# Kernel tuning notes

Hardware: AMD Instinct MI355X
Metric: run time of the kernel (lower is better)

## Reference

```python
import jax, jax.numpy as jnp
import numpy as np

B, T, C = 4, 1024, 1024
H, HKV, D = 16, 4, 64
GATE_CH = 12
ROPE_THETA = 10000.0


def _rms_norm(x):
    # F.rms_norm with default eps = machine epsilon of dtype, no learnable scale
    eps = jnp.finfo(x.dtype).eps
    ms = jnp.mean(jnp.square(x), axis=-1, keepdims=True)
    return x * jax.lax.rsqrt(ms + eps)


def _apply_rotary(x, cos, sin):
    # x: (B, T, h, D); cos/sin: (1, T, 1, D//2). Half-split rotation.
    d = x.shape[-1] // 2
    x1, x2 = x[..., :d], x[..., d:]
    y1 = x1 * cos + x2 * sin
    y2 = -x1 * sin + x2 * cos
    return jnp.concatenate([y1, y2], axis=-1)


def setup_inputs() -> dict:
    key = jax.random.key(0)
    ks = jax.random.split(key, 8)
    x = jax.random.normal(ks[0], (B, T, C), dtype=jnp.float32)
    ve = jax.random.normal(ks[1], (B, T, HKV * D), dtype=jnp.float32)
    # real RoPE tables, shape (1, T, 1, D//2)
    half = D // 2
    inv_freq = 1.0 / (ROPE_THETA ** (np.arange(half, dtype=np.float32) / half))
    freqs = np.arange(T, dtype=np.float32)[:, None] * inv_freq[None, :]
    cos = jnp.asarray(np.cos(freqs), dtype=jnp.float32).reshape(1, T, 1, half)
    sin = jnp.asarray(np.sin(freqs), dtype=jnp.float32).reshape(1, T, 1, half)
    s = 0.02
    Wq = jax.random.normal(ks[2], (H * D, C), dtype=jnp.float32) * s
    Wk = jax.random.normal(ks[3], (HKV * D, C), dtype=jnp.float32) * s
    Wv = jax.random.normal(ks[4], (HKV * D, C), dtype=jnp.float32) * s
    Wo = jax.random.normal(ks[5], (C, C), dtype=jnp.float32) * s
    Wg = jax.random.normal(ks[6], (HKV, GATE_CH), dtype=jnp.float32) * s
    return {"x": x, "ve": ve, "cos": cos, "sin": sin,
            "Wq": Wq, "Wk": Wk, "Wv": Wv, "Wo": Wo, "Wg": Wg,
            "window_size": 256}


def reference(x, ve, cos, sin, Wq, Wk, Wv, Wo, Wg, window_size):
    b, t, c = x.shape
    d = 2 * cos.shape[-1]
    h = Wq.shape[0] // d
    hkv = Wk.shape[0] // d
    rep = h // hkv

    q = (x @ Wq.T).reshape(b, t, h, d)
    k = (x @ Wk.T).reshape(b, t, hkv, d)
    v = (x @ Wv.T).reshape(b, t, hkv, d)

    # value-embedding sigmoid gate (3 * sigmoid of first 12 channels of x)
    gate = 3.0 * jax.nn.sigmoid(x[..., : Wg.shape[1]] @ Wg.T)  # (b, t, hkv)
    v = v + gate[..., None] * ve.reshape(b, t, hkv, d)

    q = _apply_rotary(q, cos, sin)
    k = _apply_rotary(k, cos, sin)
    q = _rms_norm(q) * 1.2
    k = _rms_norm(k) * 1.2

    # GQA attention with sliding-window causal mask (left=window_size, right=0)
    qg = q.reshape(b, t, hkv, rep, d)
    scale = 1.0 / jnp.sqrt(jnp.asarray(d, dtype=q.dtype))
    scores = jnp.einsum('bqgrd,bkgd->bgrqk', qg, k) * scale
    i = jnp.arange(t)[:, None]
    j = jnp.arange(t)[None, :]
    mask = (j <= i) & ((i - j) <= window_size)  # (t, t)
    scores = jnp.where(mask[None, None, None], scores, -jnp.inf)
    probs = jax.nn.softmax(scores, axis=-1)
    y = jnp.einsum('bgrqk,bkgd->bqgrd', probs, v).reshape(b, t, h * d)
    return y @ Wo.T
```

## Files before the change

### kernel.cpp

```cpp
#include <hip/hip_runtime.h>

typedef __bf16 v8bf __attribute__((ext_vector_type(8)));
typedef float v4f __attribute__((ext_vector_type(4)));
typedef unsigned int v4u __attribute__((ext_vector_type(4)));
typedef unsigned int v2u __attribute__((ext_vector_type(2)));
typedef unsigned short u16;

#define DEVI static __device__ __forceinline__

DEVI float bf2f(u16 u) {
    union { float f; unsigned int i; } c; c.i = ((unsigned int)u) << 16; return c.f;
}
DEVI u16 f2bf(float f) {
    union { float f; unsigned int i; } c; c.f = f;
    unsigned int i = c.i;
    i += 0x7fffu + ((i >> 16) & 1u);
    return (u16)(i >> 16);
}

union Frag { v4u u; v8bf v; u16 h[8]; };

#define GLD16(gptr, lptr) __builtin_amdgcn_global_load_lds( \
    (const __attribute__((address_space(1))) void*)(gptr),  \
    (__attribute__((address_space(3))) void*)(lptr), 16, 0, 0)

__global__ __launch_bounds__(256) void convert5(
    const float* __restrict__ x, const float* __restrict__ wq,
    const float* __restrict__ wk, const float* __restrict__ wv,
    const float* __restrict__ wo, u16* __restrict__ xb,
    u16* __restrict__ wb, u16* __restrict__ wob)
{
    const float* src; u16* dst; int n;
    switch (blockIdx.y) {
        case 0: src = x;  dst = xb;               n = 4096 * 1024; break;
        case 1: src = wq; dst = wb;               n = 1024 * 1024; break;
        case 2: src = wk; dst = wb + 1024 * 1024; n = 256 * 1024;  break;
        case 3: src = wv; dst = wb + 1280 * 1024; n = 256 * 1024;  break;
        default: src = wo; dst = wob;             n = 1024 * 1024; break;
    }
    const int stride = gridDim.x * 256 * 4;
    for (int i = (blockIdx.x * 256 + threadIdx.x) * 4; i < n; i += stride) {
        const float4 f = *(const float4*)(src + i);
        v2u p;
        p[0] = (unsigned int)f2bf(f.x) | ((unsigned int)f2bf(f.y) << 16);
        p[1] = (unsigned int)f2bf(f.z) | ((unsigned int)f2bf(f.w) << 16);
        *(v2u*)(dst + i) = p;
    }
}

template <bool F32OUT>
__global__ __launch_bounds__(256) void gemm_bt(
    const u16* __restrict__ A, const u16* __restrict__ B,
    void* __restrict__ Cv, int N)
{
    __shared__ __align__(16) u16 As[64 * 64];
    __shared__ __align__(16) u16 Bs[128 * 64];
    const int tid  = threadIdx.x;
    const int lane = tid & 63, l15 = lane & 15, quad = lane >> 4;
    const int w    = tid >> 6;
    const int wr   = (w >> 1) * 32, wc = (w & 1) * 64;
    const int m0   = blockIdx.y * 64, n0 = blockIdx.x * 128;

    const u16* ab = A + m0 * 1024;
    const u16* bb = B + n0 * 1024;

    const int r0 = tid >> 3;
    const int c0 = (tid & 7) * 8;
    const u16* ag = ab + r0 * 1024 + c0;
    const u16* bg = bb + r0 * 1024 + c0;
    u16* al = &As[r0 * 64 + c0];
    u16* bl = &Bs[r0 * 64 + c0];

    v4f acc[2][4];
    const v4f vzero = {0.f, 0.f, 0.f, 0.f};
#pragma unroll
    for (int i = 0; i < 2; i++)
#pragma unroll
        for (int j = 0; j < 4; j++) acc[i][j] = vzero;

    for (int k0 = 0; k0 < 1024; k0 += 64) {
        __syncthreads();
        GLD16(ag + k0,             al);
        GLD16(ag + k0 + 32 * 1024, al + 32 * 64);
        GLD16(bg + k0,             bl);
        GLD16(bg + k0 + 32 * 1024, bl + 32 * 64);
        GLD16(bg + k0 + 64 * 1024, bl + 64 * 64);
        GLD16(bg + k0 + 96 * 1024, bl + 96 * 64);
        __syncthreads();
#pragma unroll
        for (int ks = 0; ks < 2; ks++) {
            v8bf af[2];
#pragma unroll
            for (int mi = 0; mi < 2; mi++)
                af[mi] = *(const v8bf*)&As[(wr + mi * 16 + l15) * 64 + ks * 32 + quad * 8];
#pragma unroll
            for (int ni = 0; ni < 4; ni++) {
                v8bf bv = *(const v8bf*)&Bs[(wc + ni * 16 + l15) * 64 + ks * 32 + quad * 8];
#pragma unroll
                for (int mi = 0; mi < 2; mi++)
                    acc[mi][ni] = __builtin_amdgcn_mfma_f32_16x16x32_bf16(af[mi], bv, acc[mi][ni], 0, 0, 0);
            }
        }
    }
#pragma unroll
    for (int mi = 0; mi < 2; mi++) {
        const int row = m0 + wr + mi * 16 + quad * 4;
#pragma unroll
        for (int ni = 0; ni < 4; ni++) {
            const int col = n0 + wc + ni * 16 + l15;
#pragma unroll
            for (int r = 0; r < 4; r++) {
                if (F32OUT) ((float*)Cv)[(row + r) * N + col] = acc[mi][ni][r];
                else        ((u16*)Cv)[(row + r) * N + col] = f2bf(acc[mi][ni][r]);
            }
        }
    }
}

__global__ __launch_bounds__(256) void fixup(
    const u16* __restrict__ qkv, const float* __restrict__ x,
    const float* __restrict__ ve, const float* __restrict__ cs,
    const float* __restrict__ sn, const float* __restrict__ Wg,
    u16* __restrict__ qn, u16* __restrict__ kn, u16* __restrict__ vn)
{
    const int token = blockIdx.x;
    const int pos   = token & 1023;
    const int tid   = threadIdx.x;
    const int hw    = tid >> 5, l = tid & 31;
    const float c = cs[pos * 32 + l];
    const float s = sn[pos * 32 + l];
#pragma unroll
    for (int it = 0; it < 3; it++) {
        const int task = it * 8 + hw;
        if (task < 20) {
            const u16* src; u16* dst;
            if (task < 16) { src = qkv + token * 1536 + task * 64;               dst = qn + token * 1024 + task * 64; }
            else           { src = qkv + token * 1536 + 1024 + (task - 16) * 64; dst = kn + token * 256 + (task - 16) * 64; }
            const float x1 = bf2f(src[l]), x2 = bf2f(src[32 + l]);
            const float y1 = x1 * c + x2 * s;
            const float y2 = x2 * c - x1 * s;
            float ss = y1 * y1 + y2 * y2;
#pragma unroll
            for (int off = 16; off >= 1; off >>= 1) ss += __shfl_xor(ss, off, 64);
            const float inv = rsqrtf(ss * (1.0f / 64.0f) + 1.1920929e-7f) * 1.2f;
            dst[l]      = f2bf(y1 * inv);
            dst[32 + l] = f2bf(y2 * inv);
        } else {
            const int g = task - 20;
            float dot = 0.f;
#pragma unroll
            for (int cc = 0; cc < 12; cc++)
                dot += x[token * 1024 + cc] * Wg[g * 12 + cc];
            const float gate = 3.f / (1.f + __expf(-dot));
            const u16*   vsrc  = qkv + token * 1536 + 1280 + g * 64;
            const float* vesrc = ve + token * 256 + g * 64;
            u16* vdst = vn + token * 256 + g * 64;
            vdst[l]      = f2bf(bf2f(vsrc[l])      + gate * vesrc[l]);
            vdst[32 + l] = f2bf(bf2f(vsrc[32 + l]) + gate * vesrc[32 + l]);
        }
    }
}

__global__ __launch_bounds__(256) void vtrans(
    const u16* __restrict__ vn, u16* __restrict__ vt)
{
    __shared__ __align__(16) u16 T[64 * 72];
    const int tid = threadIdx.x;
    const int t0  = blockIdx.x * 64, g = blockIdx.y, b = blockIdx.z;
    {
        const int row = tid >> 2, ch = (tid & 3) * 16;
        const int goff = (b * 1024 + t0 + row) * 256 + g * 64 + ch;
        *(v4u*)&T[row * 72 + ch]     = *(const v4u*)&vn[goff];
        *(v4u*)&T[row * 72 + ch + 8] = *(const v4u*)&vn[goff + 8];
    }
    __syncthreads();
    {
        const int d = tid >> 2, tc = (tid & 3) * 16;
        Frag o0, o1;
#pragma unroll
        for (int j = 0; j < 8; j++) {
            o0.h[j] = T[(tc + j) * 72 + d];
            o1.h[j] = T[(tc + 8 + j) * 72 + d];
        }
        u16* dst = vt + ((b * 4 + g) * 64 + d) * 1024 + t0 + tc;
        *(v4u*)dst       = o0.u;
        *(v4u*)(dst + 8) = o1.u;
    }
}

__global__ __launch_bounds__(256) void attn(
    const u16* __restrict__ qn, const u16* __restrict__ kn,
    const u16* __restrict__ vt, u16* __restrict__ yo)
{
    __shared__ __align__(16) u16 Ks[64 * 72];
    __shared__ __align__(16) u16 VTs[64 * 72];
    __shared__ __align__(16) u16 Ps[4][16 * 72];
    const int tid  = threadIdx.x;
    const int w    = tid >> 6, lane = tid & 63, l15 = lane & 15, quad = lane >> 4;
    const int qb   = blockIdx.x, h = blockIdx.y, b = blockIdx.z;
    const int g    = h >> 2;
    const int qbase = qb * 64;
    const int qabs0 = qbase + w * 16;
    const int tok0  = b * 1024 + qabs0;
    u16* pw = Ps[w];

    v8bf qf[2];
#pragma unroll
    for (int ks = 0; ks < 2; ks++) {
        Frag f;
        f.u = *(const v4u*)&qn[(tok0 + l15) * 1024 + h * 64 + ks * 32 + quad * 8];
#pragma unroll
        for (int j = 0; j < 8; j++) f.h[j] = f2bf(0.125f * bf2f(f.h[j]));
        qf[ks] = f.v;
    }

    v4f o[4];
    float mi_[4], li_[4];
    const v4f vzero = {0.f, 0.f, 0.f, 0.f};
#pragma unroll
    for (int nd = 0; nd < 4; nd++) o[nd] = vzero;
#pragma unroll
    for (int r = 0; r < 4; r++) { mi_[r] = -1e30f; li_[r] = 0.f; }

    const int kstart = (qbase >= 256) ? qbase - 256 : 0;
    for (int kbase = kstart; kbase <= qbase; kbase += 64) {
        __syncthreads();
        {
            const int row = tid >> 2, ch = (tid & 3) * 16;
            const int goff = (b * 1024 + kbase + row) * 256 + g * 64 + ch;
            *(v4u*)&Ks[row * 72 + ch]     = *(const v4u*)&kn[goff];
            *(v4u*)&Ks[row * 72 + ch + 8] = *(const v4u*)&kn[goff + 8];
            const u16* vsrc = vt + ((b * 4 + g) * 64 + row) * 1024 + kbase + ch;
            *(v4u*)&VTs[row * 72 + ch]     = *(const v4u*)vsrc;
            *(v4u*)&VTs[row * 72 + ch + 8] = *(const v4u*)(vsrc + 8);
        }
        __syncthreads();

        bool skip[4], full[4];
#pragma unroll
        for (int ni = 0; ni < 4; ni++) {
            const int left = kbase + ni * 16;
            skip[ni] = (left > qabs0 + 15) || (qabs0 - (left + 15) > 256);
            full[ni] = ((left + 15) <= qabs0) && ((qabs0 + 15 - left) <= 256);
        }

        v4f sc[4];
        float rmax[4] = {-1e30f, -1e30f, -1e30f, -1e30f};
#pragma unroll
        for (int ni = 0; ni < 4; ni++) {
            if (skip[ni]) continue;
            v8bf kf0 = *(const v8bf*)&Ks[(ni * 16 + l15) * 72 + quad * 8];
            v8bf kf1 = *(const v8bf*)&Ks[(ni * 16 + l15) * 72 + 32 + quad * 8];
            v4f a = vzero;
            a = __builtin_amdgcn_mfma_f32_16x16x32_bf16(qf[0], kf0, a, 0, 0, 0);
            a = __builtin_amdgcn_mfma_f32_16x16x32_bf16(qf[1], kf1, a, 0, 0, 0);
            if (!full[ni]) {
                const int kj = kbase + ni * 16 + l15;
#pragma unroll
                for (int r = 0; r < 4; r++) {
                    const int qi = qabs0 + quad * 4 + r;
                    if (!((kj <= qi) && (qi - kj <= 256))) a[r] = -1e30f;
                }
            }
            sc[ni] = a;
#pragma unroll
            for (int r = 0; r < 4; r++) rmax[r] = fmaxf(rmax[r], a[r]);
        }
#pragma unroll
        for (int off = 8; off >= 1; off >>= 1)
#pragma unroll
            for (int r = 0; r < 4; r++)
                rmax[r] = fmaxf(rmax[r], __shfl_xor(rmax[r], off, 64));

        float mn[4], alp[4], ps[4];
#pragma unroll
        for (int r = 0; r < 4; r++) {
            mn[r]  = fmaxf(mi_[r], rmax[r]);
            alp[r] = __expf(mi_[r] - mn[r]);
            mi_[r] = mn[r];
            ps[r]  = 0.f;
        }
#pragma unroll
        for (int ni = 0; ni < 4; ni++) {
            if (skip[ni]) {
#pragma unroll
                for (int r = 0; r < 4; r++)
                    pw[(quad * 4 + r) * 72 + ni * 16 + l15] = 0;
            } else {
#pragma unroll
                for (int r = 0; r < 4; r++) {
                    const float p = __expf(sc[ni][r] - mn[r]);
                    ps[r] += p;
                    pw[(quad * 4 + r) * 72 + ni * 16 + l15] = f2bf(p);
                }
            }
        }
#pragma unroll
        for (int off = 8; off >= 1; off >>= 1)
#pragma unroll
            for (int r = 0; r < 4; r++)
                ps[r] += __shfl_xor(ps[r], off, 64);
#pragma unroll
        for (int r = 0; r < 4; r++)
            li_[r] = li_[r] * alp[r] + ps[r];
#pragma unroll
        for (int nd = 0; nd < 4; nd++)
#pragma unroll
            for (int r = 0; r < 4; r++)
                o[nd][r] *= alp[r];

#pragma unroll
        for (int ks = 0; ks < 2; ks++) {
            if (skip[2 * ks] && skip[2 * ks + 1]) continue;
            v8bf af = *(const v8bf*)&pw[l15 * 72 + ks * 32 + quad * 8];
#pragma unroll
            for (int nd = 0; nd < 4; nd++) {
                v8bf bv = *(const v8bf*)&VTs[(nd * 16 + l15) * 72 + ks * 32 + quad * 8];
                o[nd] = __builtin_amdgcn_mfma_f32_16x16x32_bf16(af, bv, o[nd], 0, 0, 0);
            }
        }
    }

    float inv[4];
#pragma unroll
    for (int r = 0; r < 4; r++) inv[r] = 1.f / li_[r];
#pragma unroll
    for (int nd = 0; nd < 4; nd++) {
        const int col = h * 64 + nd * 16 + l15;
#pragma unroll
        for (int r = 0; r < 4; r++) {
            const int row = tok0 + quad * 4 + r;
            yo[row * 1024 + col] = f2bf(o[nd][r] * inv[r]);
        }
    }
}

extern "C" void kernel_launch(void* const* d_in, const int* in_sizes, int n_in,
                              void* d_out, int out_size, void* d_ws, size_t ws_size,
                              hipStream_t stream)
{
    const float* x  = (const float*)d_in[0];
    const float* ve = (const float*)d_in[1];
    const float* cs = (const float*)d_in[2];
    const float* sn = (const float*)d_in[3];
    const float* Wq = (const float*)d_in[4];
    const float* Wk = (const float*)d_in[5];
    const float* Wv = (const float*)d_in[6];
    const float* Wo = (const float*)d_in[7];
    const float* Wg = (const float*)d_in[8];

    u16* xb  = (u16*)d_ws;
    u16* wb  = xb  + 4096 * 1024;
    u16* wob = wb  + 1536 * 1024;
    u16* qkv = wob + 1024 * 1024;
    u16* qn  = qkv + 4096 * 1536;
    u16* kn  = qn  + 4096 * 1024;
    u16* vn  = kn  + 4096 * 256;
    u16* vt  = vn  + 4096 * 256;
    u16* ay  = qkv;

    convert5<<<dim3(512, 5), 256, 0, stream>>>(x, Wq, Wk, Wv, Wo, xb, wb, wob);
    gemm_bt<false><<<dim3(12, 64), 256, 0, stream>>>(xb, wb, (void*)qkv, 1536);
    fixup<<<4096, 256, 0, stream>>>(qkv, x, ve, cs, sn, Wg, qn, kn, vn);
    vtrans<<<dim3(16, 4, 4), 256, 0, stream>>>(vn, vt);
    attn<<<dim3(16, 16, 4), 256, 0, stream>>>(qn, kn, vt, ay);
    gemm_bt<true><<<dim3(8, 64), 256, 0, stream>>>(ay, wob, d_out, 1024);
}
```

Before: 173.1 us.

## Fuse all stages into one cooperative persistent kernel with grid syncs

Replaces the six separate launches (convert, QKV GEMM, fixup, V transpose, attention, output GEMM) with a single cooperative kernel of 512 blocks. The stages are separated by grid.sync barriers. The V transpose is folded into the fixup stage through shared memory, which removes the vn intermediate buffer. The goal is to cut launch overhead and inter-kernel gaps. The cost is fixed 512-block parallelism, uneven work per stage (768 GEMM tiles over 512 blocks), grid-barrier latency, and an occupancy limit of 2 blocks per CU.

```diff
diff --git a/kernel.cpp b/kernel.cpp
--- a/kernel.cpp
+++ b/kernel.cpp
@@ -1,4 +1,7 @@
 #include <hip/hip_runtime.h>
+#include <hip/hip_cooperative_groups.h>
+
+namespace cg = cooperative_groups;
 
 typedef __bf16 v8bf __attribute__((ext_vector_type(8)));
 typedef float v4f __attribute__((ext_vector_type(4)));
@@ -24,46 +27,26 @@
     (const __attribute__((address_space(1))) void*)(gptr),  \
     (__attribute__((address_space(3))) void*)(lptr), 16, 0, 0)
 
-__global__ __launch_bounds__(256) void convert5(
-    const float* __restrict__ x, const float* __restrict__ wq,
-    const float* __restrict__ wk, const float* __restrict__ wv,
-    const float* __restrict__ wo, u16* __restrict__ xb,
-    u16* __restrict__ wb, u16* __restrict__ wob)
+DEVI void cvt4(const float* __restrict__ s, u16* __restrict__ d) {
+    const float4 f = *(const float4*)s;
+    v2u p;
+    p[0] = (unsigned int)f2bf(f.x) | ((unsigned int)f2bf(f.y) << 16);
+    p[1] = (unsigned int)f2bf(f.z) | ((unsigned int)f2bf(f.w) << 16);
+    *(v2u*)d = p;
+}
+
+DEVI void gemm_tile(const u16* __restrict__ A, const u16* __restrict__ B,
+                    void* __restrict__ Cv, int N, int m0, int n0, bool f32out,
+                    u16* smem, int tid)
 {
-    const float* src; u16* dst; int n;
-    switch (blockIdx.y) {
-        case 0: src = x;  dst = xb;               n = 4096 * 1024; break;
-        case 1: src = wq; dst = wb;               n = 1024 * 1024; break;
-        case 2: src = wk; dst = wb + 1024 * 1024; n = 256 * 1024;  break;
-        case 3: src = wv; dst = wb + 1280 * 1024; n = 256 * 1024;  break;
-        default: src = wo; dst = wob;             n = 1024 * 1024; break;
-    }
-    const int stride = gridDim.x * 256 * 4;
-    for (int i = (blockIdx.x * 256 + threadIdx.x) * 4; i < n; i += stride) {
-        const float4 f = *(const float4*)(src + i);
-        v2u p;
-        p[0] = (unsigned int)f2bf(f.x) | ((unsigned int)f2bf(f.y) << 16);
-        p[1] = (unsigned int)f2bf(f.z) | ((unsigned int)f2bf(f.w) << 16);
-        *(v2u*)(dst + i) = p;
-    }
-}
-
-template <bool F32OUT>
-__global__ __launch_bounds__(256) void gemm_bt(
-    const u16* __restrict__ A, const u16* __restrict__ B,
-    void* __restrict__ Cv, int N)
-{
-    __shared__ __align__(16) u16 As[64 * 64];
-    __shared__ __align__(16) u16 Bs[128 * 64];
-    const int tid  = threadIdx.x;
-    const int lane = tid & 63, l15 = lane & 15, quad = lane >> 4;
+    u16* As = smem;
+    u16* Bs = smem + 4096;
+    const int lane = tid & 63, l15 = lane & 15, quad = (lane >> 4) & 3;
     const int w    = tid >> 6;
     const int wr   = (w >> 1) * 32, wc = (w & 1) * 64;
-    const int m0   = blockIdx.y * 64, n0 = blockIdx.x * 128;
 
     const u16* ab = A + m0 * 1024;
     const u16* bb = B + n0 * 1024;
-
     const int r0 = tid >> 3;
     const int c0 = (tid & 7) * 8;
     const u16* ag = ab + r0 * 1024 + c0;
@@ -110,99 +93,26 @@
             const int col = n0 + wc + ni * 16 + l15;
 #pragma unroll
             for (int r = 0; r < 4; r++) {
-                if (F32OUT) ((float*)Cv)[(row + r) * N + col] = acc[mi][ni][r];
+                if (f32out) ((float*)Cv)[(row + r) * N + col] = acc[mi][ni][r];
                 else        ((u16*)Cv)[(row + r) * N + col] = f2bf(acc[mi][ni][r]);
             }
         }
     }
 }
 
-__global__ __launch_bounds__(256) void fixup(
-    const u16* __restrict__ qkv, const float* __restrict__ x,
-    const float* __restrict__ ve, const float* __restrict__ cs,
-    const float* __restrict__ sn, const float* __restrict__ Wg,
-    u16* __restrict__ qn, u16* __restrict__ kn, u16* __restrict__ vn)
+DEVI void attn_unit(const u16* __restrict__ qn, const u16* __restrict__ kn,
+                    const u16* __restrict__ vt, u16* __restrict__ yo,
+                    int u, u16* smem, int tid)
 {
-    const int token = blockIdx.x;
-    const int pos   = token & 1023;
-    const int tid   = threadIdx.x;
-    const int hw    = tid >> 5, l = tid & 31;
-    const float c = cs[pos * 32 + l];
-    const float s = sn[pos * 32 + l];
-#pragma unroll
-    for (int it = 0; it < 3; it++) {
-        const int task = it * 8 + hw;
-        if (task < 20) {
-            const u16* src; u16* dst;
-            if (task < 16) { src = qkv + token * 1536 + task * 64;               dst = qn + token * 1024 + task * 64; }
-            else           { src = qkv + token * 1536 + 1024 + (task - 16) * 64; dst = kn + token * 256 + (task - 16) * 64; }
-            const float x1 = bf2f(src[l]), x2 = bf2f(src[32 + l]);
-            const float y1 = x1 * c + x2 * s;
-            const float y2 = x2 * c - x1 * s;
-            float ss = y1 * y1 + y2 * y2;
-#pragma unroll
-            for (int off = 16; off >= 1; off >>= 1) ss += __shfl_xor(ss, off, 64);
-            const float inv = rsqrtf(ss * (1.0f / 64.0f) + 1.1920929e-7f) * 1.2f;
-            dst[l]      = f2bf(y1 * inv);
-            dst[32 + l] = f2bf(y2 * inv);
-        } else {
-            const int g = task - 20;
-            float dot = 0.f;
-#pragma unroll
-            for (int cc = 0; cc < 12; cc++)
-                dot += x[token * 1024 + cc] * Wg[g * 12 + cc];
-            const float gate = 3.f / (1.f + __expf(-dot));
-            const u16*   vsrc  = qkv + token * 1536 + 1280 + g * 64;
-            const float* vesrc = ve + token * 256 + g * 64;
-            u16* vdst = vn + token * 256 + g * 64;
-            vdst[l]      = f2bf(bf2f(vsrc[l])      + gate * vesrc[l]);
-            vdst[32 + l] = f2bf(bf2f(vsrc[32 + l]) + gate * vesrc[32 + l]);
-        }
-    }
-}
-
-__global__ __launch_bounds__(256) void vtrans(
-    const u16* __restrict__ vn, u16* __restrict__ vt)
-{
-    __shared__ __align__(16) u16 T[64 * 72];
-    const int tid = threadIdx.x;
-    const int t0  = blockIdx.x * 64, g = blockIdx.y, b = blockIdx.z;
-    {
-        const int row = tid >> 2, ch = (tid & 3) * 16;
-        const int goff = (b * 1024 + t0 + row) * 256 + g * 64 + ch;
-        *(v4u*)&T[row * 72 + ch]     = *(const v4u*)&vn[goff];
-        *(v4u*)&T[row * 72 + ch + 8] = *(const v4u*)&vn[goff + 8];
-    }
-    __syncthreads();
-    {
-        const int d = tid >> 2, tc = (tid & 3) * 16;
-        Frag o0, o1;
-#pragma unroll
-        for (int j = 0; j < 8; j++) {
-            o0.h[j] = T[(tc + j) * 72 + d];
-            o1.h[j] = T[(tc + 8 + j) * 72 + d];
-        }
-        u16* dst = vt + ((b * 4 + g) * 64 + d) * 1024 + t0 + tc;
-        *(v4u*)dst       = o0.u;
-        *(v4u*)(dst + 8) = o1.u;
-    }
-}
-
-__global__ __launch_bounds__(256) void attn(
-    const u16* __restrict__ qn, const u16* __restrict__ kn,
-    const u16* __restrict__ vt, u16* __restrict__ yo)
-{
-    __shared__ __align__(16) u16 Ks[64 * 72];
-    __shared__ __align__(16) u16 VTs[64 * 72];
-    __shared__ __align__(16) u16 Ps[4][16 * 72];
-    const int tid  = threadIdx.x;
-    const int w    = tid >> 6, lane = tid & 63, l15 = lane & 15, quad = lane >> 4;
-    const int qb   = blockIdx.x, h = blockIdx.y, b = blockIdx.z;
+    u16* Ks  = smem;
+    u16* VTs = smem + 4608;
+    const int w    = tid >> 6, lane = tid & 63, l15 = lane & 15, quad = (lane >> 4) & 3;
+    const int qb   = u & 15, h = (u >> 4) & 15, b = u >> 8;
     const int g    = h >> 2;
     const int qbase = qb * 64;
     const int qabs0 = qbase + w * 16;
     const int tok0  = b * 1024 + qabs0;
-    u16* pw = Ps[w];
+    u16* pw = smem + 9216 + w * 1152;
 
     v8bf qf[2];
 #pragma unroll
@@ -333,6 +243,99 @@
             yo[row * 1024 + col] = f2bf(o[nd][r] * inv[r]);
         }
     }
+}
+
+__global__ __launch_bounds__(256, 2) void mega(
+    const float* __restrict__ x, const float* __restrict__ ve,
+    const float* __restrict__ cs, const float* __restrict__ sn,
+    const float* __restrict__ Wq, const float* __restrict__ Wk,
+    const float* __restrict__ Wv, const float* __restrict__ Wo,
+    const float* __restrict__ Wg, float* __restrict__ out,
+    u16* __restrict__ xb, u16* __restrict__ wb, u16* __restrict__ wob,
+    u16* qkv, u16* __restrict__ qn, u16* __restrict__ kn,
+    u16* __restrict__ vt)
+{
+    __shared__ __align__(16) u16 smem[13824];
+    cg::grid_group grid = cg::this_grid();
+    const int tid = threadIdx.x;
+    const int bid = blockIdx.x;
+
+    {
+        const int base = (bid * 256 + tid) * 4;
+        const int stride = 512 * 256 * 4;
+        for (int i = base; i < 4096 * 1024; i += stride) cvt4(x + i, xb + i);
+        for (int i = base; i < 1024 * 1024; i += stride) cvt4(Wq + i, wb + i);
+        for (int i = base; i < 256 * 1024;  i += stride) cvt4(Wk + i, wb + 1024 * 1024 + i);
+        for (int i = base; i < 256 * 1024;  i += stride) cvt4(Wv + i, wb + 1280 * 1024 + i);
+        for (int i = base; i < 1024 * 1024; i += stride) cvt4(Wo + i, wob + i);
+    }
+    __threadfence();
+    grid.sync();
+
+    for (int t = bid; t < 768; t += 512)
+        gemm_tile(xb, wb, qkv, 1536, (t / 12) * 64, (t % 12) * 128, false, smem, tid);
+    __threadfence();
+    grid.sync();
+
+    {
+        u16* vbuf = smem;
+        const int token0 = bid * 8;
+        const int b = token0 >> 10;
+        const int hw = tid >> 5, l = tid & 31;
+        for (int ti = 0; ti < 8; ti++) {
+            const int token = token0 + ti;
+            const int pos   = token & 1023;
+            const float c = cs[pos * 32 + l];
+            const float s = sn[pos * 32 + l];
+#pragma unroll
+            for (int it = 0; it < 3; it++) {
+                const int task = it * 8 + hw;
+                if (task < 20) {
+                    const u16* src; u16* dst;
+                    if (task < 16) { src = qkv + token * 1536 + task * 64;               dst = qn + token * 1024 + task * 64; }
+                    else           { src = qkv + token * 1536 + 1024 + (task - 16) * 64; dst = kn + token * 256 + (task - 16) * 64; }
+                    const float x1 = bf2f(src[l]), x2 = bf2f(src[32 + l]);
+                    const float y1 = x1 * c + x2 * s;
+                    const float y2 = x2 * c - x1 * s;
+                    float ss = y1 * y1 + y2 * y2;
+#pragma unroll
+                    for (int off = 16; off >= 1; off >>= 1) ss += __shfl_xor(ss, off, 64);
+                    const float inv = rsqrtf(ss * (1.0f / 64.0f) + 1.1920929e-7f) * 1.2f;
+                    dst[l]      = f2bf(y1 * inv);
+                    dst[32 + l] = f2bf(y2 * inv);
+                } else {
+                    const int g = task - 20;
+                    float dot = 0.f;
+#pragma unroll
+                    for (int cc = 0; cc < 12; cc++)
+                        dot += x[token * 1024 + cc] * Wg[g * 12 + cc];
+                    const float gate = 3.f / (1.f + __expf(-dot));
+                    const u16*   vsrc  = qkv + token * 1536 + 1280 + g * 64;
+                    const float* vesrc = ve + token * 256 + g * 64;
+                    vbuf[ti * 256 + g * 64 + l]      = f2bf(bf2f(vsrc[l])      + gate * vesrc[l]);
+                    vbuf[ti * 256 + g * 64 + 32 + l] = f2bf(bf2f(vsrc[32 + l]) + gate * vesrc[32 + l]);
+                }
+            }
+        }
+        __syncthreads();
+        {
+            const int g = tid >> 6, d = tid & 63;
+            Frag f;
+#pragma unroll
+            for (int j = 0; j < 8; j++) f.h[j] = vbuf[j * 256 + tid];
+            u16* dst = vt + ((b * 4 + g) * 64 + d) * 1024 + (token0 & 1023);
+            *(v4u*)dst = f.u;
+        }
+    }
+    __threadfence();
+    grid.sync();
+
+    for (int u = bid; u < 1024; u += 512)
+        attn_unit(qn, kn, vt, qkv , u, smem, tid);
+    __threadfence();
+    grid.sync();
+
+    gemm_tile(qkv, wob, out, 1024, (bid >> 3) * 64, (bid & 7) * 128, true, smem, tid);
 }
 
 extern "C" void kernel_launch(void* const* d_in, const int* in_sizes, int n_in,
@@ -348,6 +351,7 @@
     const float* Wv = (const float*)d_in[6];
     const float* Wo = (const float*)d_in[7];
     const float* Wg = (const float*)d_in[8];
+    float* out = (float*)d_out;
 
     u16* xb  = (u16*)d_ws;
     u16* wb  = xb  + 4096 * 1024;
@@ -355,14 +359,9 @@
     u16* qkv = wob + 1024 * 1024;
     u16* qn  = qkv + 4096 * 1536;
     u16* kn  = qn  + 4096 * 1024;
-    u16* vn  = kn  + 4096 * 256;
-    u16* vt  = vn  + 4096 * 256;
-    u16* ay  = qkv;
-
-    convert5<<<dim3(512, 5), 256, 0, stream>>>(x, Wq, Wk, Wv, Wo, xb, wb, wob);
-    gemm_bt<false><<<dim3(12, 64), 256, 0, stream>>>(xb, wb, (void*)qkv, 1536);
-    fixup<<<4096, 256, 0, stream>>>(qkv, x, ve, cs, sn, Wg, qn, kn, vn);
-    vtrans<<<dim3(16, 4, 4), 256, 0, stream>>>(vn, vt);
-    attn<<<dim3(16, 16, 4), 256, 0, stream>>>(qn, kn, vt, ay);
-    gemm_bt<true><<<dim3(8, 64), 256, 0, stream>>>(ay, wob, d_out, 1024);
-}
+    u16* vt  = kn  + 4096 * 256;
+
+    void* args[] = { &x, &ve, &cs, &sn, &Wq, &Wk, &Wv, &Wo, &Wg, &out,
+                     &xb, &wb, &wob, &qkv, &qn, &kn, &vt };
+    hipLaunchCooperativeKernel((void*)mega, dim3(512), dim3(256), args, 0, stream);
+}
```

Result: slower. 631.4 us (+264.8%).
